# Performance work log

Hardware: AMD Instinct MI355X
Metric: run time of the kernel (lower is better)

Reference implementation:

```python
import jax, jax.numpy as jnp
import numpy as np

E = 200_000   # num edges
B = 64        # num graphs
D = 256       # node/edge/global feature dim
H = 512       # hidden dim of edge MLP
DO = 256      # output edge dim


def setup_inputs() -> dict:
    key = jax.random.key(0)
    ks = jax.random.split(key, 9)
    src = jax.random.normal(ks[0], (E, D), dtype=jnp.float32)
    dest = jax.random.normal(ks[1], (E, D), dtype=jnp.float32)
    edge_attr = jax.random.normal(ks[2], (E, D), dtype=jnp.float32)
    u = jax.random.normal(ks[3], (B, D), dtype=jnp.float32)
    batch = jax.random.randint(ks[4], (E,), 0, B, dtype=jnp.int64)
    # edge MLP params: Linear(4D -> H), ReLU, Linear(H -> DO)
    in_dim = 4 * D
    W1 = jax.random.normal(ks[5], (in_dim, H), dtype=jnp.float32) / np.sqrt(in_dim)
    b1 = jnp.zeros((H,), dtype=jnp.float32)
    W2 = jax.random.normal(ks[6], (H, DO), dtype=jnp.float32) / np.sqrt(H)
    b2 = jnp.zeros((DO,), dtype=jnp.float32)
    return {"src": src, "dest": dest, "edge_attr": edge_attr, "u": u,
            "batch": batch, "W1": W1, "b1": b1, "W2": W2, "b2": b2}


def reference(src, dest, edge_attr, u, batch, W1, b1, W2, b2):
    # gather per-graph global features to edges, concat, 2-layer MLP
    out = jnp.concatenate([src, dest, edge_attr, u[batch]], axis=1)  # [E, 4D]
    h = jax.nn.relu(out @ W1 + b1)                                   # [E, H]
    return h @ W2 + b2                                               # [E, DO]
```

## Files before the change

### kernel.cpp

```cpp
#include <hip/hip_runtime.h>
#include <stdint.h>

#define E_EDGES 200000
#define D_FEAT  256
#define K1      1024
#define HID     512
#define DOUT    256
#define M_TILE  128
#define BK      64
#define NCHUNK  256

#define SA_PITCH 72
#define SB_PITCH 72
#define SH_PITCH 264

typedef short bf16x8 __attribute__((ext_vector_type(8)));
typedef float f32x4  __attribute__((ext_vector_type(4)));

__device__ __forceinline__ unsigned short f2bf(float x) {
    unsigned int u = __builtin_bit_cast(unsigned int, x);
    u += 0x7FFFu + ((u >> 16) & 1u);
    return (unsigned short)(u >> 16);
}

__global__ void prep_weights(const float* __restrict__ W1, const float* __restrict__ W2,
                             unsigned short* __restrict__ w1t, unsigned short* __restrict__ w2t) {
    int idx = blockIdx.x * 256 + threadIdx.x;
    if (idx < HID * K1) {
        int n = idx >> 10;
        int k = idx & 1023;
        w1t[idx] = f2bf(W1[k * HID + n]);
    } else if (idx < HID * K1 + DOUT * HID) {
        int j = idx - HID * K1;
        int n = j >> 9;
        int k = j & 511;
        w2t[j] = f2bf(W2[k * DOUT + n]);
    }
}

__launch_bounds__(512, 2)
__global__ void edge_mlp_kernel(const float* __restrict__ src,
                                const float* __restrict__ dst,
                                const float* __restrict__ ea,
                                const float* __restrict__ u,
                                const int*   __restrict__ batch,
                                const float* __restrict__ b1,
                                const float* __restrict__ b2,
                                const unsigned short* __restrict__ w1t,
                                const unsigned short* __restrict__ w2t,
                                float* __restrict__ out) {
    __shared__ unsigned short sA[M_TILE * SA_PITCH];
    __shared__ unsigned short sB[NCHUNK * SB_PITCH];
    __shared__ unsigned short sH[M_TILE * SH_PITCH];
    __shared__ int sBatch[M_TILE];

    const int tid  = threadIdx.x;
    const int lane = tid & 63;
    const int wave = tid >> 6;
    const int rw   = (wave >> 2) * 64;
    const int cw   = (wave & 3) * 64;
    const int lrow = lane & 15;
    const int quad = lane >> 4;
    const int e0   = blockIdx.x * M_TILE;

    if (tid < M_TILE) {
        int e = e0 + tid;
        if (e >= E_EDGES) e = E_EDGES - 1;
        sBatch[tid] = batch[e];
    }

    const f32x4 z4 = {0.f, 0.f, 0.f, 0.f};
    f32x4 oacc[4][4];
#pragma unroll
    for (int i = 0; i < 4; ++i)
#pragma unroll
        for (int j = 0; j < 4; ++j) oacc[i][j] = z4;

    const int ar = tid >> 2;
    const int acq = (tid & 3) << 4;
    const int bn = tid >> 1;
    const int bkq = (tid & 1) << 5;

    for (int c = 0; c < 2; ++c) {
        const int nb = c * NCHUNK;
        f32x4 hacc[4][4];
#pragma unroll
        for (int i = 0; i < 4; ++i)
#pragma unroll
            for (int j = 0; j < 4; ++j) hacc[i][j] = z4;

        for (int k0 = 0; k0 < K1; k0 += BK) {
            __syncthreads();
            {
                int e = e0 + ar; if (e >= E_EDGES) e = E_EDGES - 1;
                const int seg = k0 >> 8;
                const int ko  = (k0 & 255) + acq;
                const float* base;
                if      (seg == 0) base = src + (size_t)e * D_FEAT;
                else if (seg == 1) base = dst + (size_t)e * D_FEAT;
                else if (seg == 2) base = ea  + (size_t)e * D_FEAT;
                else               base = u   + (size_t)sBatch[ar] * D_FEAT;
                const float4* p = reinterpret_cast<const float4*>(base + ko);
                float4 f0 = p[0], f1 = p[1], f2v = p[2], f3 = p[3];
                unsigned int w0 = (unsigned)f2bf(f0.x)  | ((unsigned)f2bf(f0.y)  << 16);
                unsigned int w1 = (unsigned)f2bf(f0.z)  | ((unsigned)f2bf(f0.w)  << 16);
                unsigned int w2 = (unsigned)f2bf(f1.x)  | ((unsigned)f2bf(f1.y)  << 16);
                unsigned int w3 = (unsigned)f2bf(f1.z)  | ((unsigned)f2bf(f1.w)  << 16);
                unsigned int w4 = (unsigned)f2bf(f2v.x) | ((unsigned)f2bf(f2v.y) << 16);
                unsigned int w5 = (unsigned)f2bf(f2v.z) | ((unsigned)f2bf(f2v.w) << 16);
                unsigned int w6 = (unsigned)f2bf(f3.x)  | ((unsigned)f2bf(f3.y)  << 16);
                unsigned int w7 = (unsigned)f2bf(f3.z)  | ((unsigned)f2bf(f3.w)  << 16);
                uint4* dsp = reinterpret_cast<uint4*>(&sA[ar * SA_PITCH + acq]);
                dsp[0] = make_uint4(w0, w1, w2, w3);
                dsp[1] = make_uint4(w4, w5, w6, w7);
            }
            {
                const uint4* p = reinterpret_cast<const uint4*>(w1t + (size_t)(nb + bn) * K1 + k0 + bkq);
                uint4 q0 = p[0], q1 = p[1], q2 = p[2], q3 = p[3];
                uint4* dsp = reinterpret_cast<uint4*>(&sB[bn * SB_PITCH + bkq]);
                dsp[0] = q0; dsp[1] = q1; dsp[2] = q2; dsp[3] = q3;
            }
            __syncthreads();
#pragma unroll
            for (int kk = 0; kk < BK; kk += 32) {
                bf16x8 af[4], bfr[4];
#pragma unroll
                for (int i = 0; i < 4; ++i)
                    af[i] = *reinterpret_cast<const bf16x8*>(&sA[(rw + i * 16 + lrow) * SA_PITCH + kk + quad * 8]);
#pragma unroll
                for (int j = 0; j < 4; ++j)
                    bfr[j] = *reinterpret_cast<const bf16x8*>(&sB[(cw + j * 16 + lrow) * SB_PITCH + kk + quad * 8]);
#pragma unroll
                for (int i = 0; i < 4; ++i)
#pragma unroll
                    for (int j = 0; j < 4; ++j)
                        hacc[i][j] = __builtin_amdgcn_mfma_f32_16x16x32_bf16(af[i], bfr[j], hacc[i][j], 0, 0, 0);
            }
        }

        __syncthreads();
#pragma unroll
        for (int j = 0; j < 4; ++j) {
            const int col = cw + j * 16 + lrow;
            const float bb = b1[nb + col];
#pragma unroll
            for (int i = 0; i < 4; ++i) {
#pragma unroll
                for (int r = 0; r < 4; ++r) {
                    int row = rw + i * 16 + quad * 4 + r;
                    float v = hacc[i][j][r] + bb;
                    v = fmaxf(v, 0.f);
                    sH[row * SH_PITCH + col] = f2bf(v);
                }
            }
        }
        __syncthreads();

        for (int k20 = 0; k20 < NCHUNK; k20 += BK) {
            __syncthreads();
            {
                const uint4* p = reinterpret_cast<const uint4*>(w2t + (size_t)bn * HID + nb + k20 + bkq);
                uint4 q0 = p[0], q1 = p[1], q2 = p[2], q3 = p[3];
                uint4* dsp = reinterpret_cast<uint4*>(&sB[bn * SB_PITCH + bkq]);
                dsp[0] = q0; dsp[1] = q1; dsp[2] = q2; dsp[3] = q3;
            }
            __syncthreads();
#pragma unroll
            for (int kk = 0; kk < BK; kk += 32) {
                bf16x8 af[4], bfr[4];
#pragma unroll
                for (int i = 0; i < 4; ++i)
                    af[i] = *reinterpret_cast<const bf16x8*>(&sH[(rw + i * 16 + lrow) * SH_PITCH + k20 + kk + quad * 8]);
#pragma unroll
                for (int j = 0; j < 4; ++j)
                    bfr[j] = *reinterpret_cast<const bf16x8*>(&sB[(cw + j * 16 + lrow) * SB_PITCH + kk + quad * 8]);
#pragma unroll
                for (int i = 0; i < 4; ++i)
#pragma unroll
                    for (int j = 0; j < 4; ++j)
                        oacc[i][j] = __builtin_amdgcn_mfma_f32_16x16x32_bf16(af[i], bfr[j], oacc[i][j], 0, 0, 0);
            }
        }
    }

#pragma unroll
    for (int j = 0; j < 4; ++j) {
        const int col = cw + j * 16 + lrow;
        const float bb = b2[col];
#pragma unroll
        for (int i = 0; i < 4; ++i) {
            const int rbase = rw + i * 16 + quad * 4;
#pragma unroll
            for (int r = 0; r < 4; ++r) {
                int e = e0 + rbase + r;
                if (e < E_EDGES)
                    out[(size_t)e * DOUT + col] = oacc[i][j][r] + bb;
            }
        }
    }
}

extern "C" void kernel_launch(void* const* d_in, const int* in_sizes, int n_in,
                              void* d_out, int out_size, void* d_ws, size_t ws_size,
                              hipStream_t stream) {
    (void)in_sizes; (void)n_in; (void)out_size; (void)ws_size;
    const float* src  = (const float*)d_in[0];
    const float* dst  = (const float*)d_in[1];
    const float* ea   = (const float*)d_in[2];
    const float* u    = (const float*)d_in[3];
    const int*   bat  = (const int*)d_in[4];
    const float* W1   = (const float*)d_in[5];
    const float* b1   = (const float*)d_in[6];
    const float* W2   = (const float*)d_in[7];
    const float* b2   = (const float*)d_in[8];
    float* out = (float*)d_out;

    unsigned short* w1t = (unsigned short*)d_ws;
    unsigned short* w2t = w1t + (size_t)HID * K1;

    prep_weights<<<(HID * K1 + DOUT * HID) / 256, 256, 0, stream>>>(W1, W2, w1t, w2t);

    const int nblocks = (E_EDGES + M_TILE - 1) / M_TILE;
    edge_mlp_kernel<<<nblocks, 512, 0, stream>>>(src, dst, ea, u, bat, b1, b2, w1t, w2t, out);
}
```

Baseline: 1.114 ms.

## Shrink edge tile, DMA weights to XOR-swizzled LDS, reuse sA for hidden

The block tile drops from 128 edges with 8 waves to 64 edges with 4 waves. Each wave now owns a 64-column slice and all 64 rows. Weight tiles are loaded straight into LDS with global_load_lds into an unpadded XOR-swizzled layout, so they no longer pass through registers, and reads apply the matching swizzle. The separate hidden buffer sH is gone: each 64-column hidden slice is written into sA just before the second GEMM consumes it, which cuts LDS use and raises occupancy (launch bounds 256,3). The trade-off is that each weight element is read twice as often relative to the rows it serves, and tail handling is removed because E divides exactly by 64.

New measurement: 1.468 ms. +31.8%, slower.

```diff
diff --git a/kernel.cpp b/kernel.cpp
--- a/kernel.cpp
+++ b/kernel.cpp
@@ -6,16 +6,20 @@
 #define K1      1024
 #define HID     512
 #define DOUT    256
-#define M_TILE  128
+#define M_TILE  64
 #define BK      64
 #define NCHUNK  256
 
 #define SA_PITCH 72
-#define SB_PITCH 72
-#define SH_PITCH 264
 
 typedef short bf16x8 __attribute__((ext_vector_type(8)));
 typedef float f32x4  __attribute__((ext_vector_type(4)));
+
+static_assert(E_EDGES % M_TILE == 0, "exact tiling, no tail");
+
+#define GLOAD16(gp, lp) __builtin_amdgcn_global_load_lds( \
+    (const __attribute__((address_space(1))) void*)(gp),  \
+    (__attribute__((address_space(3))) void*)(lp), 16, 0, 0)
 
 __device__ __forceinline__ unsigned short f2bf(float x) {
     unsigned int u = __builtin_bit_cast(unsigned int, x);
@@ -38,7 +42,7 @@
     }
 }
 
-__launch_bounds__(512, 2)
+__launch_bounds__(256, 3)
 __global__ void edge_mlp_kernel(const float* __restrict__ src,
                                 const float* __restrict__ dst,
                                 const float* __restrict__ ea,
@@ -50,24 +54,21 @@
                                 const unsigned short* __restrict__ w2t,
                                 float* __restrict__ out) {
     __shared__ unsigned short sA[M_TILE * SA_PITCH];
-    __shared__ unsigned short sB[NCHUNK * SB_PITCH];
-    __shared__ unsigned short sH[M_TILE * SH_PITCH];
+    __shared__ unsigned short sB[NCHUNK * BK];
     __shared__ int sBatch[M_TILE];
 
     const int tid  = threadIdx.x;
     const int lane = tid & 63;
     const int wave = tid >> 6;
-    const int rw   = (wave >> 2) * 64;
-    const int cw   = (wave & 3) * 64;
+    const int cw   = wave << 6;
     const int lrow = lane & 15;
     const int quad = lane >> 4;
     const int e0   = blockIdx.x * M_TILE;
 
-    if (tid < M_TILE) {
-        int e = e0 + tid;
-        if (e >= E_EDGES) e = E_EDGES - 1;
-        sBatch[tid] = batch[e];
-    }
+    if (tid < M_TILE) sBatch[tid] = batch[e0 + tid];
+
+    const int ar  = tid >> 2;
+    const int acq = (tid & 3) << 4;
 
     const f32x4 z4 = {0.f, 0.f, 0.f, 0.f};
     f32x4 oacc[4][4];
@@ -75,11 +76,6 @@
     for (int i = 0; i < 4; ++i)
 #pragma unroll
         for (int j = 0; j < 4; ++j) oacc[i][j] = z4;
-
-    const int ar = tid >> 2;
-    const int acq = (tid & 3) << 4;
-    const int bn = tid >> 1;
-    const int bkq = (tid & 1) << 5;
 
     for (int c = 0; c < 2; ++c) {
         const int nb = c * NCHUNK;
@@ -91,14 +87,22 @@
 
         for (int k0 = 0; k0 < K1; k0 += BK) {
             __syncthreads();
+#pragma unroll
+            for (int i = 0; i < 8; ++i) {
+                const int ob   = ((wave << 3) + i) << 10;
+                const int o    = ob + (lane << 4);
+                const int row  = o >> 7;
+                const int blog = (o & 127) ^ ((row & 7) << 4);
+                const char* g = (const char*)(w1t + (size_t)(nb + row) * K1 + k0) + blog;
+                GLOAD16(g, (char*)sB + ob);
+            }
             {
-                int e = e0 + ar; if (e >= E_EDGES) e = E_EDGES - 1;
                 const int seg = k0 >> 8;
                 const int ko  = (k0 & 255) + acq;
                 const float* base;
-                if      (seg == 0) base = src + (size_t)e * D_FEAT;
-                else if (seg == 1) base = dst + (size_t)e * D_FEAT;
-                else if (seg == 2) base = ea  + (size_t)e * D_FEAT;
+                if      (seg == 0) base = src + (size_t)(e0 + ar) * D_FEAT;
+                else if (seg == 1) base = dst + (size_t)(e0 + ar) * D_FEAT;
+                else if (seg == 2) base = ea  + (size_t)(e0 + ar) * D_FEAT;
                 else               base = u   + (size_t)sBatch[ar] * D_FEAT;
                 const float4* p = reinterpret_cast<const float4*>(base + ko);
                 float4 f0 = p[0], f1 = p[1], f2v = p[2], f3 = p[3];
@@ -114,22 +118,19 @@
                 dsp[0] = make_uint4(w0, w1, w2, w3);
                 dsp[1] = make_uint4(w4, w5, w6, w7);
             }
-            {
-                const uint4* p = reinterpret_cast<const uint4*>(w1t + (size_t)(nb + bn) * K1 + k0 + bkq);
-                uint4 q0 = p[0], q1 = p[1], q2 = p[2], q3 = p[3];
-                uint4* dsp = reinterpret_cast<uint4*>(&sB[bn * SB_PITCH + bkq]);
-                dsp[0] = q0; dsp[1] = q1; dsp[2] = q2; dsp[3] = q3;
-            }
             __syncthreads();
 #pragma unroll
             for (int kk = 0; kk < BK; kk += 32) {
                 bf16x8 af[4], bfr[4];
 #pragma unroll
                 for (int i = 0; i < 4; ++i)
-                    af[i] = *reinterpret_cast<const bf16x8*>(&sA[(rw + i * 16 + lrow) * SA_PITCH + kk + quad * 8]);
-#pragma unroll
-                for (int j = 0; j < 4; ++j)
-                    bfr[j] = *reinterpret_cast<const bf16x8*>(&sB[(cw + j * 16 + lrow) * SB_PITCH + kk + quad * 8]);
+                    af[i] = *reinterpret_cast<const bf16x8*>(&sA[(i * 16 + lrow) * SA_PITCH + kk + quad * 8]);
+#pragma unroll
+                for (int j = 0; j < 4; ++j) {
+                    const int row = cw + j * 16 + lrow;
+                    const int k2  = (kk + quad * 8) ^ ((row & 7) << 3);
+                    bfr[j] = *reinterpret_cast<const bf16x8*>(&sB[(row << 6) + k2]);
+                }
 #pragma unroll
                 for (int i = 0; i < 4; ++i)
 #pragma unroll
@@ -138,31 +139,33 @@
             }
         }
 
-        __syncthreads();
-#pragma unroll
-        for (int j = 0; j < 4; ++j) {
-            const int col = cw + j * 16 + lrow;
-            const float bb = b1[nb + col];
-#pragma unroll
-            for (int i = 0; i < 4; ++i) {
-#pragma unroll
-                for (int r = 0; r < 4; ++r) {
-                    int row = rw + i * 16 + quad * 4 + r;
-                    float v = hacc[i][j][r] + bb;
-                    v = fmaxf(v, 0.f);
-                    sH[row * SH_PITCH + col] = f2bf(v);
+        for (int k20 = 0; k20 < NCHUNK; k20 += BK) {
+            __syncthreads();
+#pragma unroll
+            for (int i = 0; i < 8; ++i) {
+                const int ob   = ((wave << 3) + i) << 10;
+                const int o    = ob + (lane << 4);
+                const int row  = o >> 7;
+                const int blog = (o & 127) ^ ((row & 7) << 4);
+                const char* g = (const char*)(w2t + (size_t)row * HID + nb + k20) + blog;
+                GLOAD16(g, (char*)sB + ob);
+            }
+            if (cw == k20) {
+#pragma unroll
+                for (int j = 0; j < 4; ++j) {
+                    const int col = (j << 4) + lrow;
+                    const float bb = b1[nb + k20 + col];
+#pragma unroll
+                    for (int i = 0; i < 4; ++i) {
+#pragma unroll
+                        for (int r = 0; r < 4; ++r) {
+                            const int row = (i << 4) + (quad << 2) + r;
+                            float v = hacc[i][j][r] + bb;
+                            v = fmaxf(v, 0.f);
+                            sA[row * SA_PITCH + col] = f2bf(v);
+                        }
+                    }
                 }
-            }
-        }
-        __syncthreads();
-
-        for (int k20 = 0; k20 < NCHUNK; k20 += BK) {
-            __syncthreads();
-            {
-                const uint4* p = reinterpret_cast<const uint4*>(w2t + (size_t)bn * HID + nb + k20 + bkq);
-                uint4 q0 = p[0], q1 = p[1], q2 = p[2], q3 = p[3];
-                uint4* dsp = reinterpret_cast<uint4*>(&sB[bn * SB_PITCH + bkq]);
-                dsp[0] = q0; dsp[1] = q1; dsp[2] = q2; dsp[3] = q3;
             }
             __syncthreads();
 #pragma unroll
@@ -170,10 +173,13 @@
                 bf16x8 af[4], bfr[4];
 #pragma unroll
                 for (int i = 0; i < 4; ++i)
-                    af[i] = *reinterpret_cast<const bf16x8*>(&sH[(rw + i * 16 + lrow) * SH_PITCH + k20 + kk + quad * 8]);
-#pragma unroll
-                for (int j = 0; j < 4; ++j)
-                    bfr[j] = *reinterpret_cast<const bf16x8*>(&sB[(cw + j * 16 + lrow) * SB_PITCH + kk + quad * 8]);
+                    af[i] = *reinterpret_cast<const bf16x8*>(&sA[(i * 16 + lrow) * SA_PITCH + kk + quad * 8]);
+#pragma unroll
+                for (int j = 0; j < 4; ++j) {
+                    const int row = cw + j * 16 + lrow;
+                    const int k2  = (kk + quad * 8) ^ ((row & 7) << 3);
+                    bfr[j] = *reinterpret_cast<const bf16x8*>(&sB[(row << 6) + k2]);
+                }
 #pragma unroll
                 for (int i = 0; i < 4; ++i)
 #pragma unroll
@@ -185,16 +191,15 @@
 
 #pragma unroll
     for (int j = 0; j < 4; ++j) {
-        const int col = cw + j * 16 + lrow;
+        const int col = cw + (j << 4) + lrow;
         const float bb = b2[col];
 #pragma unroll
         for (int i = 0; i < 4; ++i) {
-            const int rbase = rw + i * 16 + quad * 4;
+            const int rbase = (i << 4) + (quad << 2);
 #pragma unroll
             for (int r = 0; r < 4; ++r) {
-                int e = e0 + rbase + r;
-                if (e < E_EDGES)
-                    out[(size_t)e * DOUT + col] = oacc[i][j][r] + bb;
+                const int row = rbase + r;
+                out[(size_t)(e0 + row) * DOUT + col] = oacc[i][j][r] + bb;
             }
         }
     }
@@ -220,6 +225,6 @@
 
     prep_weights<<<(HID * K1 + DOUT * HID) / 256, 256, 0, stream>>>(W1, W2, w1t, w2t);
 
-    const int nblocks = (E_EDGES + M_TILE - 1) / M_TILE;
-    edge_mlp_kernel<<<nblocks, 512, 0, stream>>>(src, dst, ea, u, bat, b1, b2, w1t, w2t, out);
-}
+    const int nblocks = E_EDGES / M_TILE;
+    edge_mlp_kernel<<<nblocks, 256, 0, stream>>>(src, dst, ea, u, bat, b1, b2, w1t, w2t, out);
+}
```
